# Kernel tuning notes

Hardware: AMD Instinct MI355X
Metric: run time of the kernel (lower is better)

## Reference

```python
import jax, jax.numpy as jnp
import numpy as np

IN = 4096      # in_channels (unpacked)
OUT = 11008    # out_channels
GROUP = 128    # quantization group size
W_BIT = 4
PACK = 32 // W_BIT  # 8 int4 values per int32
N_GROUPS = IN // GROUP
BATCH = 64


def setup_inputs() -> dict:
    key = jax.random.key(0)
    k1, k2, k3, k4 = jax.random.split(key, 4)
    x = jax.random.normal(k1, (BATCH, IN), dtype=jnp.float32)
    # bit-packed int4 weights: 8 nibbles per int32, packed along input dim
    qweight = jax.random.randint(k2, (IN // PACK, OUT), 0, jnp.iinfo(jnp.int32).max, dtype=jnp.int32)
    scales = jax.random.uniform(k3, (N_GROUPS, OUT), dtype=jnp.float32) * 0.01 + 1e-3
    # zero points near mid-range of int4
    zeros = 7.5 + jax.random.uniform(k4, (N_GROUPS, OUT), dtype=jnp.float32) - 0.5
    g_idx = (jnp.arange(IN) // GROUP).astype(jnp.int32)
    return {"x": x, "qweight": qweight, "scales": scales, "zeros": zeros, "g_idx": g_idx}


def unpack_int4(qweight):
    # [IN//8, OUT] int32 -> [IN, OUT] float32 in [0, 15]
    shifts = (jnp.arange(PACK, dtype=jnp.int32) * W_BIT)  # [8]
    nibbles = (qweight[:, None, :] >> shifts[None, :, None]) & 0xF  # [IN//8, 8, OUT]
    return nibbles.reshape(IN, OUT).astype(jnp.float32)


def reference(x, qweight, scales, zeros, g_idx):
    w_int = unpack_int4(qweight)                       # [IN, OUT]
    W = (w_int - zeros[g_idx]) * scales[g_idx]         # group-wise dequant, [IN, OUT]
    return x @ W                                       # [BATCH, OUT]
```

## Files before the change

### kernel.cpp

```cpp
#include <hip/hip_runtime.h>
#include <stdint.h>


#define IN 4096
#define OUT 11008
#define BATCH 64
#define SPLITK 8
#define KSPL (IN / SPLITK)
#define BN 128
#define BK 64
#define NBLK (OUT / BN)
#define LDR 72

typedef __attribute__((ext_vector_type(8))) __bf16 bf16x8;
typedef __attribute__((ext_vector_type(4))) float f32x4;

static __device__ __forceinline__ ushort f2bf(float f) {
  uint32_t u = __float_as_uint(f);
  u += 0x7fff + ((u >> 16) & 1);
  return (ushort)(u >> 16);
}

__global__ void cvt_x_kernel(const float* __restrict__ x, ushort* __restrict__ xbf) {
  int gid = blockIdx.x * blockDim.x + threadIdx.x;
  float4 v = ((const float4*)x)[gid];
  ushort4 o;
  o.x = f2bf(v.x); o.y = f2bf(v.y); o.z = f2bf(v.z); o.w = f2bf(v.w);
  ((ushort4*)xbf)[gid] = o;
}

__global__ __launch_bounds__(256, 2) void mpq_gemm(
    const ushort* __restrict__ xbf,
    const int* __restrict__ qweight,
    const float* __restrict__ scales,
    const float* __restrict__ zeros,
    float* __restrict__ out)
{
  __shared__ ushort At[64 * LDR];
  __shared__ ushort Bt[128 * LDR];

  const int n0 = blockIdx.x * BN;
  const int k0 = blockIdx.y * KSPL;

  const int tid = threadIdx.x;
  const int lane = tid & 63;
  const int w = tid >> 6;
  const int wm = w >> 1, wn = w & 1;
  const int mlane = lane & 15, quad = lane >> 4;

  const int rA = tid >> 2;
  const int kA = (tid & 3) * 16;
  const int rB = tid >> 5;
  const int ncol = tid & 31;

  f32x4 acc[2][4] = {};

  for (int kc = k0; kc < k0 + KSPL; kc += BK) {
    const int g = kc >> 7;

    const uint4* asrc = (const uint4*)(xbf + rA * IN + kc + kA);
    uint4 a0 = asrc[0];
    uint4 a1 = asrc[1];

    int qv[4];
    float sv[4], zv[4];
    const int qrow = (kc >> 3) + rB;
#pragma unroll
    for (int c = 0; c < 4; ++c) {
      int n = ncol + 32 * c;
      qv[c] = qweight[qrow * OUT + n0 + n];
      sv[c] = scales[g * OUT + n0 + n];
      zv[c] = zeros[g * OUT + n0 + n];
    }

    __syncthreads();

    *(uint4*)&At[rA * LDR + kA] = a0;
    *(uint4*)&At[rA * LDR + kA + 8] = a1;

#pragma unroll
    for (int c = 0; c < 4; ++c) {
      const float s = sv[c];
      const float nzs = -zv[c] * s;
      const uint32_t q = (uint32_t)qv[c];
      ushort ob[8];
#pragma unroll
      for (int j = 0; j < 8; ++j) {
        float wf = (float)((q >> (4 * j)) & 0xF);
        ob[j] = f2bf(fmaf(wf, s, nzs));
      }
      *(uint4*)&Bt[(ncol + 32 * c) * LDR + rB * 8] = *(uint4*)ob;
    }

    __syncthreads();

#pragma unroll
    for (int ks = 0; ks < BK; ks += 32) {
      bf16x8 af[2], bfr[4];
#pragma unroll
      for (int i = 0; i < 2; ++i)
        af[i] = *(const bf16x8*)&At[(32 * wm + 16 * i + mlane) * LDR + ks + quad * 8];
#pragma unroll
      for (int j = 0; j < 4; ++j)
        bfr[j] = *(const bf16x8*)&Bt[(64 * wn + 16 * j + mlane) * LDR + ks + quad * 8];
#pragma unroll
      for (int i = 0; i < 2; ++i)
#pragma unroll
        for (int j = 0; j < 4; ++j)
          acc[i][j] = __builtin_amdgcn_mfma_f32_16x16x32_bf16(af[i], bfr[j], acc[i][j], 0, 0, 0);
    }
  }

#pragma unroll
  for (int i = 0; i < 2; ++i) {
    const int mbase = 32 * wm + 16 * i + quad * 4;
#pragma unroll
    for (int j = 0; j < 4; ++j) {
      const int col = n0 + 64 * wn + 16 * j + mlane;
#pragma unroll
      for (int r = 0; r < 4; ++r) {
        atomicAdd(&out[(mbase + r) * OUT + col], acc[i][j][r]);
      }
    }
  }
}

extern "C" void kernel_launch(void* const* d_in, const int* in_sizes, int n_in,
                              void* d_out, int out_size, void* d_ws, size_t ws_size,
                              hipStream_t stream) {
  const float* x = (const float*)d_in[0];
  const int* qweight = (const int*)d_in[1];
  const float* scales = (const float*)d_in[2];
  const float* zeros = (const float*)d_in[3];
  float* out = (float*)d_out;
  ushort* xbf = (ushort*)d_ws;

  hipMemsetAsync(d_out, 0, (size_t)BATCH * OUT * sizeof(float), stream);
  cvt_x_kernel<<<256, 256, 0, stream>>>(x, xbf);
  dim3 grid(NBLK, SPLITK);
  mpq_gemm<<<grid, 256, 0, stream>>>(xbf, qweight, scales, zeros, out);
}
```

Before: 106.0 us.

## Move group dequant out of inner loop via magic-bias bf16 and x-sum correction

Builds bf16 weights directly from nibbles with the 0x4300 magic-bias trick (value 128+q), dropping the per-element convert and fma. The per-group scale and zero are applied once per accumulator after each group, using precomputed per-row x group sums that the x-conversion kernel now produces. Launch bounds raise the occupancy target to 3 blocks. This trades per-element dequant ALU work for extra accumulator registers, a per-group epilogue, and possible precision loss from subtracting large 128-biased terms.

```diff
diff --git a/kernel.cpp b/kernel.cpp
--- a/kernel.cpp
+++ b/kernel.cpp
@@ -20,27 +20,44 @@
   u += 0x7fff + ((u >> 16) & 1);
   return (ushort)(u >> 16);
 }
+static __device__ __forceinline__ float bf2f(ushort h) {
+  return __uint_as_float(((uint32_t)h) << 16);
+}
 
-__global__ void cvt_x_kernel(const float* __restrict__ x, ushort* __restrict__ xbf) {
+__global__ void cvt_xsum_kernel(const float* __restrict__ x, ushort* __restrict__ xbf,
+                                float* __restrict__ xsum) {
   int gid = blockIdx.x * blockDim.x + threadIdx.x;
   float4 v = ((const float4*)x)[gid];
   ushort4 o;
   o.x = f2bf(v.x); o.y = f2bf(v.y); o.z = f2bf(v.z); o.w = f2bf(v.w);
   ((ushort4*)xbf)[gid] = o;
+  float s = bf2f(o.x) + bf2f(o.y) + bf2f(o.z) + bf2f(o.w);
+#pragma unroll
+  for (int m = 1; m <= 16; m <<= 1) s += __shfl_xor(s, m);
+  int lane = threadIdx.x & 63;
+  if ((lane & 31) == 0) {
+    int k4 = gid * 4;
+    int m = k4 >> 12;
+    int g = (k4 & 4095) >> 7;
+    xsum[g * 64 + m] = s;
+  }
 }
 
-__global__ __launch_bounds__(256, 2) void mpq_gemm(
+__global__ __launch_bounds__(256, 3) void mpq_gemm(
     const ushort* __restrict__ xbf,
     const int* __restrict__ qweight,
     const float* __restrict__ scales,
     const float* __restrict__ zeros,
+    const float* __restrict__ xsum,
     float* __restrict__ out)
 {
   __shared__ ushort At[64 * LDR];
   __shared__ ushort Bt[128 * LDR];
+  __shared__ float xs[4 * 64];
 
   const int n0 = blockIdx.x * BN;
   const int k0 = blockIdx.y * KSPL;
+  const int g0 = k0 >> 7;
 
   const int tid = threadIdx.x;
   const int lane = tid & 63;
@@ -48,66 +65,91 @@
   const int wm = w >> 1, wn = w & 1;
   const int mlane = lane & 15, quad = lane >> 4;
 
+  xs[tid] = xsum[(g0 + (tid >> 6)) * 64 + (tid & 63)];
+
   const int rA = tid >> 2;
   const int kA = (tid & 3) * 16;
   const int rB = tid >> 5;
   const int ncol = tid & 31;
 
-  f32x4 acc[2][4] = {};
+  f32x4 macc[2][4] = {};
 
-  for (int kc = k0; kc < k0 + KSPL; kc += BK) {
-    const int g = kc >> 7;
-
-    const uint4* asrc = (const uint4*)(xbf + rA * IN + kc + kA);
-    uint4 a0 = asrc[0];
-    uint4 a1 = asrc[1];
-
-    int qv[4];
-    float sv[4], zv[4];
-    const int qrow = (kc >> 3) + rB;
+  for (int gl = 0; gl < 4; ++gl) {
+    const int g = g0 + gl;
+    float sj[4], zj[4];
 #pragma unroll
-    for (int c = 0; c < 4; ++c) {
-      int n = ncol + 32 * c;
-      qv[c] = qweight[qrow * OUT + n0 + n];
-      sv[c] = scales[g * OUT + n0 + n];
-      zv[c] = zeros[g * OUT + n0 + n];
+    for (int j = 0; j < 4; ++j) {
+      const int col = n0 + 64 * wn + 16 * j + mlane;
+      sj[j] = scales[g * OUT + col];
+      zj[j] = zeros[g * OUT + col];
     }
 
-    __syncthreads();
-
-    *(uint4*)&At[rA * LDR + kA] = a0;
-    *(uint4*)&At[rA * LDR + kA + 8] = a1;
+    f32x4 gacc[2][4] = {};
 
 #pragma unroll
-    for (int c = 0; c < 4; ++c) {
-      const float s = sv[c];
-      const float nzs = -zv[c] * s;
-      const uint32_t q = (uint32_t)qv[c];
-      ushort ob[8];
+    for (int cc = 0; cc < 2; ++cc) {
+      const int kc = k0 + gl * 128 + cc * 64;
+
+      const uint4* asrc = (const uint4*)(xbf + rA * IN + kc + kA);
+      uint4 a0 = asrc[0];
+      uint4 a1 = asrc[1];
+
+      int qv[4];
+      const int qrow = (kc >> 3) + rB;
 #pragma unroll
-      for (int j = 0; j < 8; ++j) {
-        float wf = (float)((q >> (4 * j)) & 0xF);
-        ob[j] = f2bf(fmaf(wf, s, nzs));
+      for (int c = 0; c < 4; ++c)
+        qv[c] = qweight[qrow * OUT + n0 + ncol + 32 * c];
+
+      __syncthreads();
+
+      *(uint4*)&At[rA * LDR + kA] = a0;
+      *(uint4*)&At[rA * LDR + kA + 8] = a1;
+
+#pragma unroll
+      for (int c = 0; c < 4; ++c) {
+        const uint32_t q = (uint32_t)qv[c];
+        uint32_t p[4];
+#pragma unroll
+        for (int j = 0; j < 4; ++j) {
+          p[j] = 0x43004300u | ((q >> (8 * j)) & 0xFu) | (((q >> (8 * j + 4)) & 0xFu) << 16);
+        }
+        *(uint4*)&Bt[(ncol + 32 * c) * LDR + rB * 8] = *(uint4*)p;
       }
-      *(uint4*)&Bt[(ncol + 32 * c) * LDR + rB * 8] = *(uint4*)ob;
+
+      __syncthreads();
+
+#pragma unroll
+      for (int ks = 0; ks < BK; ks += 32) {
+        bf16x8 af[2], bfr[4];
+#pragma unroll
+        for (int i = 0; i < 2; ++i)
+          af[i] = *(const bf16x8*)&At[(32 * wm + 16 * i + mlane) * LDR + ks + quad * 8];
+#pragma unroll
+        for (int j = 0; j < 4; ++j)
+          bfr[j] = *(const bf16x8*)&Bt[(64 * wn + 16 * j + mlane) * LDR + ks + quad * 8];
+#pragma unroll
+        for (int i = 0; i < 2; ++i)
+#pragma unroll
+          for (int j = 0; j < 4; ++j)
+            gacc[i][j] = __builtin_amdgcn_mfma_f32_16x16x32_bf16(af[i], bfr[j], gacc[i][j], 0, 0, 0);
+      }
     }
 
-    __syncthreads();
-
 #pragma unroll
-    for (int ks = 0; ks < BK; ks += 32) {
-      bf16x8 af[2], bfr[4];
+    for (int j = 0; j < 4; ++j) {
+      const float uj = sj[j] * (128.0f + zj[j]);
 #pragma unroll
-      for (int i = 0; i < 2; ++i)
-        af[i] = *(const bf16x8*)&At[(32 * wm + 16 * i + mlane) * LDR + ks + quad * 8];
+      for (int i = 0; i < 2; ++i) {
+        const int mbase = 32 * wm + 16 * i + quad * 4;
 #pragma unroll
-      for (int j = 0; j < 4; ++j)
-        bfr[j] = *(const bf16x8*)&Bt[(64 * wn + 16 * j + mlane) * LDR + ks + quad * 8];
-#pragma unroll
-      for (int i = 0; i < 2; ++i)
-#pragma unroll
-        for (int j = 0; j < 4; ++j)
-          acc[i][j] = __builtin_amdgcn_mfma_f32_16x16x32_bf16(af[i], bfr[j], acc[i][j], 0, 0, 0);
+        for (int r = 0; r < 4; ++r) {
+          const float S = xs[gl * 64 + mbase + r];
+          float acc = macc[i][j][r];
+          acc = fmaf(sj[j], gacc[i][j][r], acc);
+          acc = fmaf(-uj, S, acc);
+          macc[i][j][r] = acc;
+        }
+      }
     }
   }
 
@@ -118,9 +160,8 @@
     for (int j = 0; j < 4; ++j) {
       const int col = n0 + 64 * wn + 16 * j + mlane;
 #pragma unroll
-      for (int r = 0; r < 4; ++r) {
-        atomicAdd(&out[(mbase + r) * OUT + col], acc[i][j][r]);
-      }
+      for (int r = 0; r < 4; ++r)
+        atomicAdd(&out[(mbase + r) * OUT + col], macc[i][j][r]);
     }
   }
 }
@@ -134,9 +175,10 @@
   const float* zeros = (const float*)d_in[3];
   float* out = (float*)d_out;
   ushort* xbf = (ushort*)d_ws;
+  float* xsum = (float*)((char*)d_ws + (1 << 19));
 
   hipMemsetAsync(d_out, 0, (size_t)BATCH * OUT * sizeof(float), stream);
-  cvt_x_kernel<<<256, 256, 0, stream>>>(x, xbf);
+  cvt_xsum_kernel<<<256, 256, 0, stream>>>(x, xbf, xsum);
   dim3 grid(NBLK, SPLITK);
-  mpq_gemm<<<grid, 256, 0, stream>>>(xbf, qweight, scales, zeros, out);
+  mpq_gemm<<<grid, 256, 0, stream>>>(xbf, qweight, scales, zeros, xsum, out);
 }
```

Measured after the change: 103.6 us. 1.02x faster.
